# Performance work log

Hardware: AMD Instinct MI355X
Metric: run time of the kernel (lower is better)

The kernel has to match this reference:

```python
import jax, jax.numpy as jnp
import numpy as np
from jax import lax

B, T, I, H, L = 64, 512, 256, 512, 2


def setup_inputs() -> dict:
    key = jax.random.key(0)
    ks = jax.random.split(key, 5)
    s_in = (6.0 / (H + I)) ** 0.5   # xavier-uniform-like scale
    s_hh = (6.0 / (H + H)) ** 0.5
    return {
        "x": jax.random.normal(ks[0], (B, T, I), jnp.float32),
        "h_0": jnp.zeros((L, B, H), jnp.float32),
        "W_ih_0": jax.random.normal(ks[1], (H, I), jnp.float32) * s_in,
        "W_hh_0": jax.random.normal(ks[2], (H, H), jnp.float32) * s_hh,
        "b_ih_0": jnp.zeros((H,), jnp.float32),
        "b_hh_0": jnp.zeros((H,), jnp.float32),
        "W_ih_1": jax.random.normal(ks[3], (H, H), jnp.float32) * s_hh,
        "W_hh_1": jax.random.normal(ks[4], (H, H), jnp.float32) * s_hh,
        "b_ih_1": jnp.zeros((H,), jnp.float32),
        "b_hh_1": jnp.zeros((H,), jnp.float32),
    }


def _rnn_layer(xs, h0, W_ih, W_hh, b_ih, b_hh):
    # Precompute the input-to-hidden projection for all timesteps at once
    # (same math as per-step F.linear, just batched): [B,T,H]
    xW = jnp.einsum('bti,hi->bth', xs, W_ih) + b_ih + b_hh

    def step(h, xw_t):  # h:[B,H], xw_t:[B,H]
        h_new = jnp.tanh(xw_t + h @ W_hh.T)
        return h_new, h_new

    h_last, ys = lax.scan(step, h0, jnp.swapaxes(xW, 0, 1))  # ys: [T,B,H]
    return jnp.swapaxes(ys, 0, 1), h_last


def reference(x, h_0, W_ih_0, W_hh_0, b_ih_0, b_hh_0,
              W_ih_1, W_hh_1, b_ih_1, b_hh_1):
    out0, h_n0 = _rnn_layer(x, h_0[0], W_ih_0, W_hh_0, b_ih_0, b_hh_0)
    out1, h_n1 = _rnn_layer(out0, h_0[1], W_ih_1, W_hh_1, b_ih_1, b_hh_1)
    h_n = jnp.stack([h_n0, h_n1], axis=0)  # [L,B,H]
    return out1, h_n
```

## Files before the change

kernel.cpp:

```cpp
#include <hip/hip_runtime.h>


#define kB 64
#define kT 512
#define kI 256
#define kH 512
#define kBH (kB * kH)

typedef _Float16 half8 __attribute__((ext_vector_type(8)));
typedef float floatx4 __attribute__((ext_vector_type(4)));

constexpr size_t W16_B   = 0;
constexpr size_t OUT0M_B = 16u * 1024 * 1024;
constexpr size_t H1M_B   = OUT0M_B + (size_t)(kT + 1) * kBH * 2;
constexpr size_t CNT_B   = H1M_B + (size_t)(kT + 1) * kBH * 2;

__device__ inline half8 cvt8(const float* p) {
    const float4* p4 = (const float4*)p;
    float4 a = p4[0], b = p4[1];
    half8 h;
    h[0] = (_Float16)a.x; h[1] = (_Float16)a.y; h[2] = (_Float16)a.z; h[3] = (_Float16)a.w;
    h[4] = (_Float16)b.x; h[5] = (_Float16)b.y; h[6] = (_Float16)b.z; h[7] = (_Float16)b.w;
    return h;
}

__device__ inline void sc_store_half(_Float16* p, _Float16 v) {
    unsigned short u = __builtin_bit_cast(unsigned short, v);
    __hip_atomic_store((unsigned short*)p, u, __ATOMIC_RELAXED, __HIP_MEMORY_SCOPE_AGENT);
}

__device__ inline void wait_slot(const int* p, int target) {
    int guard = 0;
    while (__hip_atomic_load(p, __ATOMIC_RELAXED, __HIP_MEMORY_SCOPE_AGENT) < target)
        if (++guard > 100000000) break;
    asm volatile("" ::: "memory");
}

__device__ inline void wait_pair(const int* slots, int target) {
    const int* p = slots + (threadIdx.x & 1);
    int guard = 0;
    for (;;) {
        int v = __hip_atomic_load(p, __ATOMIC_RELAXED, __HIP_MEMORY_SCOPE_AGENT);
        if (__all(v >= target)) break;
        if (++guard > 100000000) break;
    }
    asm volatile("" ::: "memory");
}

__device__ inline void wait_quarters(const int* slots, int own, int target) {
    const int idx = threadIdx.x & 3;
    const int* p = slots + idx;
    int guard = 0;
    for (;;) {
        int v = (idx == own) ? target
              : __hip_atomic_load(p, __ATOMIC_RELAXED, __HIP_MEMORY_SCOPE_AGENT);
        if (__all(v >= target)) break;
        if (++guard > 100000000) break;
    }
    asm volatile("" ::: "memory");
}

__global__ void setup_kernel(const float* __restrict__ h0, const float* __restrict__ wih0,
                             _Float16* __restrict__ out0m, _Float16* __restrict__ h1m,
                             _Float16* __restrict__ w16, int* __restrict__ cnt) {
    int idx = blockIdx.x * blockDim.x + threadIdx.x;
    if (idx < kBH) out0m[idx] = (_Float16)h0[idx];
    else if (idx < 2 * kBH) h1m[idx - kBH] = (_Float16)h0[idx];
    w16[idx] = (_Float16)wih0[idx];
    if (idx < 256) cnt[idx] = 0;
}

__global__ __launch_bounds__(256) void xw_kernel(
    const float* __restrict__ x, const _Float16* __restrict__ w16,
    const float* __restrict__ bih, const float* __restrict__ bhh, float* xw) {
    const int mb = blockIdx.x >> 3, nb = blockIdx.x & 7;
    const int wave = threadIdx.x >> 6, lane = threadIdx.x & 63;
    const int r = lane & 15, q = lane >> 4;
    const int m0 = mb * 64 + wave * 16;
    half8 a[8];
#pragma unroll
    for (int ko = 0; ko < 8; ++ko)
        a[ko] = cvt8(x + (size_t)(m0 + r) * kI + ko * 32 + q * 8);
#pragma unroll
    for (int ct = 0; ct < 4; ++ct) {
        const int cc = nb * 64 + ct * 16 + r;
        const float bias = bih[cc] + bhh[cc];
        floatx4 acc = {bias, bias, bias, bias};
#pragma unroll
        for (int ko = 0; ko < 8; ++ko) {
            half8 b = *(const half8*)(w16 + (size_t)cc * kI + ko * 32 + q * 8);
            acc = __builtin_amdgcn_mfma_f32_16x16x32_f16(a[ko], b, acc, 0, 0, 0);
        }
#pragma unroll
        for (int j = 0; j < 4; ++j)
            xw[(size_t)(m0 + q * 4 + j) * kH + cc] = acc[j];
    }
}

__global__ __launch_bounds__(1024) void scan_kernel(
    const float* xw,
    _Float16* __restrict__ out0m, _Float16* __restrict__ h1m,
    int* __restrict__ slots0, int* __restrict__ slots1,
    float* out1,
    const float* __restrict__ whh0,
    const float* __restrict__ wih1, const float* __restrict__ whh1,
    const float* __restrict__ bih1, const float* __restrict__ bhh1) {
    __shared__ __align__(16) char smem[40960];

    const int blk = blockIdx.x;
    const int tid = threadIdx.x;
    const int wave = tid >> 6, lane = tid & 63;
    const int r = lane & 15, q = lane >> 4;
    const int rb = (r << 10), swz = (r & 7) << 4;

    if (blk < 8) {
        const int g = blk >> 1, half = blk & 1;
        const int b0 = g * 16;
        const int cc = half * 256 + wave * 16 + r;
        half8 wfh[16];
#pragma unroll
        for (int ks = 0; ks < 16; ++ks)
            wfh[ks] = cvt8(whh0 + (size_t)cc * kH + ks * 32 + q * 8);
        int* myslot = slots0 + g * 2 + half;
        const int* peerslot = slots0 + g * 2 + (half ^ 1);
        const int srow = tid >> 6, sunit = tid & 63;
        const size_t sg_off = (size_t)(b0 + srow) * kH + sunit * 8;
        char* sdst = smem + (((srow << 10) | (sunit << 4)) ^ ((srow & 7) << 4));

        for (int t = 0; t < kT; ++t) {
            float xwv[4];
#pragma unroll
            for (int j = 0; j < 4; ++j)
                xwv[j] = xw[((size_t)(b0 + q * 4 + j) * kT + t) * kH + cc];
            if (t > 0) wait_slot(peerslot, t);
            *(half8*)sdst = *(const half8*)(out0m + (size_t)t * kBH + sg_off);
            __syncthreads();
            floatx4 acc = {0.f, 0.f, 0.f, 0.f};
#pragma unroll
            for (int ks = 0; ks < 16; ++ks) {
                half8 la = *(const half8*)(smem + ((rb | (ks << 6) | (q << 4)) ^ swz));
                acc = __builtin_amdgcn_mfma_f32_16x16x32_f16(la, wfh[ks], acc, 0, 0, 0);
            }
            _Float16* dst = out0m + (size_t)(t + 1) * kBH + (size_t)(b0 + q * 4) * kH + cc;
#pragma unroll
            for (int j = 0; j < 4; ++j)
                sc_store_half(dst + (size_t)j * kH, (_Float16)tanhf(acc[j] + xwv[j]));
            asm volatile("" ::: "memory");
            __builtin_amdgcn_s_waitcnt(0x0F70);
            __syncthreads();
            if (tid == 0)
                __hip_atomic_store(myslot, t + 1, __ATOMIC_RELAXED, __HIP_MEMORY_SCOPE_AGENT);
        }
    } else {
        const int b2 = blk - 8;
        const int g = b2 >> 2, qb = b2 & 3;
        const int b0 = g * 16;
        const int ct = wave >> 1, part = wave & 1;
        const int cc = qb * 128 + ct * 16 + r;
        half8 wf[16];
        const float* wsrc = part ? wih1 : whh1;
#pragma unroll
        for (int ks = 0; ks < 16; ++ks)
            wf[ks] = cvt8(wsrc + (size_t)cc * kH + ks * 32 + q * 8);
        const float bias = (part == 0) ? (bih1[cc] + bhh1[cc]) : 0.f;
        int* myslot = slots1 + g * 4 + qb;
        const int* gq = slots1 + g * 4;
        const int* gh = slots0 + g * 2;
        const int u = ct * 64 + lane;
        const int srow = u >> 5, sunit = u & 31;
        const size_t sg_off = (size_t)(b0 + srow) * kH + sunit * 16;
        const int tbase = part ? 16384 : 0;
        char* sd0 = smem + tbase + ((((srow << 10) | (sunit << 5))) ^ ((srow & 7) << 4));
        char* sd1 = smem + tbase + ((((srow << 10) | (sunit << 5)) | 16) ^ ((srow & 7) << 4));
        float* redp = (float*)(smem + 32768) + (ct * 256 + lane * 4);

        for (int t = 0; t < kT; ++t) {
            const _Float16* sl;
            if (part == 0) {
                if (t > 0) wait_quarters(gq, qb, t);
                sl = h1m + (size_t)t * kBH;
            } else {
                wait_pair(gh, t + 1);
                sl = out0m + (size_t)(t + 1) * kBH;
            }
            half8 s0 = *(const half8*)(sl + sg_off);
            half8 s1 = *(const half8*)(sl + sg_off + 8);
            *(half8*)sd0 = s0;
            *(half8*)sd1 = s1;
            __syncthreads();
            floatx4 acc = {0.f, 0.f, 0.f, 0.f};
            const char* tb = smem + tbase;
#pragma unroll
            for (int ks = 0; ks < 16; ++ks) {
                half8 la = *(const half8*)(tb + ((rb | (ks << 6) | (q << 4)) ^ swz));
                acc = __builtin_amdgcn_mfma_f32_16x16x32_f16(la, wf[ks], acc, 0, 0, 0);
            }
            if (part == 1) *(floatx4*)redp = acc;
            __syncthreads();
            if (part == 0) {
                floatx4 o = *(const floatx4*)redp;
#pragma unroll
                for (int j = 0; j < 4; ++j) {
                    float v = tanhf(acc[j] + o[j] + bias);
                    out1[((size_t)(b0 + q * 4 + j) * kT + t) * kH + cc] = v;
                    sc_store_half(h1m + (size_t)(t + 1) * kBH + (size_t)(b0 + q * 4 + j) * kH + cc,
                                  (_Float16)v);
                }
            }
            asm volatile("" ::: "memory");
            __builtin_amdgcn_s_waitcnt(0x0F70);
            __syncthreads();
            if (tid == 0)
                __hip_atomic_store(myslot, t + 1, __ATOMIC_RELAXED, __HIP_MEMORY_SCOPE_AGENT);
        }
    }
}

__global__ void finalize_kernel(const _Float16* __restrict__ out0m,
                                const _Float16* __restrict__ h1m,
                                float* __restrict__ out) {
    int idx = blockIdx.x * blockDim.x + threadIdx.x;
    float* hn = out + (size_t)kB * kT * kH;
    if (idx < kBH) hn[idx] = (float)out0m[(size_t)kT * kBH + idx];
    else hn[idx] = (float)h1m[(size_t)kT * kBH + (idx - kBH)];
}

extern "C" void kernel_launch(void* const* d_in, const int* in_sizes, int n_in,
                              void* d_out, int out_size, void* d_ws, size_t ws_size,
                              hipStream_t stream) {
    const float* x    = (const float*)d_in[0];
    const float* h0in = (const float*)d_in[1];
    const float* wih0 = (const float*)d_in[2];
    const float* whh0 = (const float*)d_in[3];
    const float* bih0 = (const float*)d_in[4];
    const float* bhh0 = (const float*)d_in[5];
    const float* wih1 = (const float*)d_in[6];
    const float* whh1 = (const float*)d_in[7];
    const float* bih1 = (const float*)d_in[8];
    const float* bhh1 = (const float*)d_in[9];
    float* out = (float*)d_out;
    char* ws = (char*)d_ws;

    _Float16* w16   = (_Float16*)(ws + W16_B);
    _Float16* out0m = (_Float16*)(ws + OUT0M_B);
    _Float16* h1m   = (_Float16*)(ws + H1M_B);
    int* cnt        = (int*)(ws + CNT_B);
    int* slots0 = cnt;
    int* slots1 = cnt + 32;

    setup_kernel<<<512, 256, 0, stream>>>(h0in, wih0, out0m, h1m, w16, cnt);
    xw_kernel<<<4096, 256, 0, stream>>>(x, w16, bih0, bhh0, out);
    scan_kernel<<<24, 1024, 0, stream>>>(out, out0m, h1m, slots0, slots1, out,
                                         whh0, wih1, whh1, bih1, bhh1);
    finalize_kernel<<<256, 256, 0, stream>>>(out0m, h1m, out);
}
```

Before: 2.046 ms.

## Replace counter-slot handshakes with sentinel-polled LLC loads and double-buffered LDS state

Removes the per-step atomic slot counters and barriers used to signal progress between workgroups. Hidden-state buffers are pre-filled with an all-ones sentinel, and consumers poll the data itself through cache-bypassing loads until no sentinel remains. Each workgroup keeps its own half or quarter of the state in double-buffered LDS, so only the peer's portion is fetched from memory, and block size is halved with each wave computing more columns. Also switches to an exp-based tanh and pre-converts the weights to fp16 in setup. This risks subtle memory-ordering bugs, and a legitimate fp16 value of 0xFFFF would never occur, but NaN-like patterns could stall polling.

```diff
diff --git a/kernel.cpp b/kernel.cpp
--- a/kernel.cpp
+++ b/kernel.cpp
@@ -9,11 +9,63 @@
 
 typedef _Float16 half8 __attribute__((ext_vector_type(8)));
 typedef float floatx4 __attribute__((ext_vector_type(4)));
+typedef unsigned u32x4 __attribute__((ext_vector_type(4)));
+typedef unsigned u32x2 __attribute__((ext_vector_type(2)));
+
+#define MFMA(a, b, c) __builtin_amdgcn_mfma_f32_16x16x32_f16(a, b, c, 0, 0, 0)
 
 constexpr size_t W16_B   = 0;
-constexpr size_t OUT0M_B = 16u * 1024 * 1024;
+constexpr size_t WH0_B   = 256u * 1024;
+constexpr size_t WI1_B   = WH0_B + 512u * 1024;
+constexpr size_t WH1_B   = WI1_B + 512u * 1024;
+constexpr size_t OUT0M_B = 2u * 1024 * 1024;
 constexpr size_t H1M_B   = OUT0M_B + (size_t)(kT + 1) * kBH * 2;
-constexpr size_t CNT_B   = H1M_B + (size_t)(kT + 1) * kBH * 2;
+
+__device__ inline void llc_store16(void* p, u32x4 v) {
+    asm volatile("global_store_dwordx4 %0, %1, off sc0 sc1" :: "v"(p), "v"(v) : "memory");
+}
+__device__ inline void llc_store8(void* p, u32x2 v) {
+    asm volatile("global_store_dwordx2 %0, %1, off sc0 sc1" :: "v"(p), "v"(v) : "memory");
+}
+#define LLC_ISSUE16(dst, p) \
+    asm volatile("global_load_dwordx4 %0, %1, off sc0 sc1" : "=v"(dst) : "v"(p))
+
+__device__ inline unsigned dirty4(u32x4 v) {
+    unsigned m01 = v[0] > v[1] ? v[0] : v[1];
+    unsigned m23 = v[2] > v[3] ? v[2] : v[3];
+    unsigned m = m01 > m23 ? m01 : m23;
+    return m == 0xFFFFFFFFu;
+}
+
+__device__ inline float fast_tanh(float x) {
+    float e = __expf(2.f * x);
+    return 1.f - 2.f / (e + 1.f);
+}
+
+__global__ void setup_kernel(const float* __restrict__ h0,
+                             const float* __restrict__ wih0, const float* __restrict__ whh0,
+                             const float* __restrict__ wih1, const float* __restrict__ whh1,
+                             _Float16* __restrict__ w16, _Float16* __restrict__ wh0_16,
+                             _Float16* __restrict__ wi1_16, _Float16* __restrict__ wh1_16,
+                             _Float16* __restrict__ out0m, _Float16* __restrict__ h1m) {
+    size_t tid = (size_t)blockIdx.x * blockDim.x + threadIdx.x;
+    size_t stride = (size_t)gridDim.x * blockDim.x;
+    for (size_t i = tid; i < (size_t)kH * kI; i += stride) w16[i] = (_Float16)wih0[i];
+    for (size_t i = tid; i < (size_t)kH * kH; i += stride) {
+        wh0_16[i] = (_Float16)whh0[i];
+        wi1_16[i] = (_Float16)wih1[i];
+        wh1_16[i] = (_Float16)whh1[i];
+    }
+    for (size_t i = tid; i < kBH; i += stride) {
+        out0m[i] = (_Float16)h0[i];
+        h1m[i]   = (_Float16)h0[kBH + i];
+    }
+    u32x4 s = {0xFFFFFFFFu, 0xFFFFFFFFu, 0xFFFFFFFFu, 0xFFFFFFFFu};
+    u32x4* a = (u32x4*)(out0m + kBH);
+    u32x4* b = (u32x4*)(h1m + kBH);
+    const size_t nf = (size_t)kT * kBH / 8;
+    for (size_t i = tid; i < nf; i += stride) { a[i] = s; b[i] = s; }
+}
 
 __device__ inline half8 cvt8(const float* p) {
     const float4* p4 = (const float4*)p;
@@ -22,52 +74,6 @@
     h[0] = (_Float16)a.x; h[1] = (_Float16)a.y; h[2] = (_Float16)a.z; h[3] = (_Float16)a.w;
     h[4] = (_Float16)b.x; h[5] = (_Float16)b.y; h[6] = (_Float16)b.z; h[7] = (_Float16)b.w;
     return h;
-}
-
-__device__ inline void sc_store_half(_Float16* p, _Float16 v) {
-    unsigned short u = __builtin_bit_cast(unsigned short, v);
-    __hip_atomic_store((unsigned short*)p, u, __ATOMIC_RELAXED, __HIP_MEMORY_SCOPE_AGENT);
-}
-
-__device__ inline void wait_slot(const int* p, int target) {
-    int guard = 0;
-    while (__hip_atomic_load(p, __ATOMIC_RELAXED, __HIP_MEMORY_SCOPE_AGENT) < target)
-        if (++guard > 100000000) break;
-    asm volatile("" ::: "memory");
-}
-
-__device__ inline void wait_pair(const int* slots, int target) {
-    const int* p = slots + (threadIdx.x & 1);
-    int guard = 0;
-    for (;;) {
-        int v = __hip_atomic_load(p, __ATOMIC_RELAXED, __HIP_MEMORY_SCOPE_AGENT);
-        if (__all(v >= target)) break;
-        if (++guard > 100000000) break;
-    }
-    asm volatile("" ::: "memory");
-}
-
-__device__ inline void wait_quarters(const int* slots, int own, int target) {
-    const int idx = threadIdx.x & 3;
-    const int* p = slots + idx;
-    int guard = 0;
-    for (;;) {
-        int v = (idx == own) ? target
-              : __hip_atomic_load(p, __ATOMIC_RELAXED, __HIP_MEMORY_SCOPE_AGENT);
-        if (__all(v >= target)) break;
-        if (++guard > 100000000) break;
-    }
-    asm volatile("" ::: "memory");
-}
-
-__global__ void setup_kernel(const float* __restrict__ h0, const float* __restrict__ wih0,
-                             _Float16* __restrict__ out0m, _Float16* __restrict__ h1m,
-                             _Float16* __restrict__ w16, int* __restrict__ cnt) {
-    int idx = blockIdx.x * blockDim.x + threadIdx.x;
-    if (idx < kBH) out0m[idx] = (_Float16)h0[idx];
-    else if (idx < 2 * kBH) h1m[idx - kBH] = (_Float16)h0[idx];
-    w16[idx] = (_Float16)wih0[idx];
-    if (idx < 256) cnt[idx] = 0;
 }
 
 __global__ __launch_bounds__(256) void xw_kernel(
@@ -89,7 +95,7 @@
 #pragma unroll
         for (int ko = 0; ko < 8; ++ko) {
             half8 b = *(const half8*)(w16 + (size_t)cc * kI + ko * 32 + q * 8);
-            acc = __builtin_amdgcn_mfma_f32_16x16x32_f16(a[ko], b, acc, 0, 0, 0);
+            acc = MFMA(a[ko], b, acc);
         }
 #pragma unroll
         for (int j = 0; j < 4; ++j)
@@ -97,121 +103,190 @@
     }
 }
 
-__global__ __launch_bounds__(1024) void scan_kernel(
+__global__ __launch_bounds__(512, 2) void scan_kernel(
     const float* xw,
     _Float16* __restrict__ out0m, _Float16* __restrict__ h1m,
-    int* __restrict__ slots0, int* __restrict__ slots1,
     float* out1,
-    const float* __restrict__ whh0,
-    const float* __restrict__ wih1, const float* __restrict__ whh1,
+    const _Float16* __restrict__ wh0_16,
+    const _Float16* __restrict__ wi1_16, const _Float16* __restrict__ wh1_16,
     const float* __restrict__ bih1, const float* __restrict__ bhh1) {
-    __shared__ __align__(16) char smem[40960];
+    __shared__ __align__(16) char smem[24576];
 
     const int blk = blockIdx.x;
     const int tid = threadIdx.x;
     const int wave = tid >> 6, lane = tid & 63;
     const int r = lane & 15, q = lane >> 4;
-    const int rb = (r << 10), swz = (r & 7) << 4;
+    const int swzr = (r & 7) << 4;
+    const int srow = tid >> 5, sl32 = tid & 31;
+    const int swzs = (srow & 7) << 4;
 
     if (blk < 8) {
         const int g = blk >> 1, half = blk & 1;
         const int b0 = g * 16;
-        const int cc = half * 256 + wave * 16 + r;
-        half8 wfh[16];
-#pragma unroll
-        for (int ks = 0; ks < 16; ++ks)
-            wfh[ks] = cvt8(whh0 + (size_t)cc * kH + ks * 32 + q * 8);
-        int* myslot = slots0 + g * 2 + half;
-        const int* peerslot = slots0 + g * 2 + (half ^ 1);
-        const int srow = tid >> 6, sunit = tid & 63;
-        const size_t sg_off = (size_t)(b0 + srow) * kH + sunit * 8;
-        char* sdst = smem + (((srow << 10) | (sunit << 4)) ^ ((srow & 7) << 4));
+        const int cb = half * 256 + wave * 32;
+        half8 wf0[16], wf1[16];
+#pragma unroll
+        for (int ks = 0; ks < 16; ++ks) {
+            wf0[ks] = *(const half8*)(wh0_16 + (size_t)(cb + r) * kH + ks * 32 + q * 8);
+            wf1[ks] = *(const half8*)(wh0_16 + (size_t)(cb + 16 + r) * kH + ks * 32 + q * 8);
+        }
+        {
+            u32x4 v = *(const u32x4*)(out0m + (size_t)(b0 + srow) * kH + half * 256 + sl32 * 8);
+            *(u32x4*)(smem + srow * 512 + ((sl32 * 16) ^ swzs)) = v;
+        }
+        __syncthreads();
 
         for (int t = 0; t < kT; ++t) {
-            float xwv[4];
-#pragma unroll
-            for (int j = 0; j < 4; ++j)
-                xwv[j] = xw[((size_t)(b0 + q * 4 + j) * kT + t) * kH + cc];
-            if (t > 0) wait_slot(peerslot, t);
-            *(half8*)sdst = *(const half8*)(out0m + (size_t)t * kBH + sg_off);
+            char* bufR = smem + (t & 1) * 8192;
+            char* bufW = smem + ((t + 1) & 1) * 8192;
+            float xv0[4], xv1[4];
+#pragma unroll
+            for (int j = 0; j < 4; ++j) {
+                const size_t rowb = ((size_t)(b0 + q * 4 + j) * kT + t) * kH;
+                xv0[j] = xw[rowb + cb + r];
+                xv1[j] = xw[rowb + cb + 16 + r];
+            }
+            u32x4 ph[8];
+            const _Float16* pb = out0m + (size_t)t * kBH + (size_t)(b0 + r) * kH
+                                 + (half ^ 1) * 256 + q * 8;
+#pragma unroll
+            for (int i = 0; i < 8; ++i) LLC_ISSUE16(ph[i], pb + i * 32);
+            floatx4 a0 = {0.f, 0.f, 0.f, 0.f}, a1 = {0.f, 0.f, 0.f, 0.f};
+#pragma unroll
+            for (int i = 0; i < 8; ++i) {
+                half8 la = *(const half8*)(bufR + r * 512 + ((i * 64 + q * 16) ^ swzr));
+                a0 = MFMA(la, wf0[half * 8 + i], a0);
+                a1 = MFMA(la, wf1[half * 8 + i], a1);
+            }
+            {
+                int guard = 0;
+                for (;;) {
+                    __builtin_amdgcn_s_waitcnt(0x0F70);
+                    __builtin_amdgcn_sched_barrier(0);
+                    unsigned d = 0;
+#pragma unroll
+                    for (int i = 0; i < 8; ++i) d |= dirty4(ph[i]);
+                    if (!__any(d != 0)) break;
+                    if (++guard > (1 << 20)) break;
+#pragma unroll
+                    for (int i = 0; i < 8; ++i) LLC_ISSUE16(ph[i], pb + i * 32);
+                }
+            }
+#pragma unroll
+            for (int i = 0; i < 8; ++i) {
+                half8 pa = __builtin_bit_cast(half8, ph[i]);
+                a0 = MFMA(pa, wf0[(half ^ 1) * 8 + i], a0);
+                a1 = MFMA(pa, wf1[(half ^ 1) * 8 + i], a1);
+            }
+#pragma unroll
+            for (int j = 0; j < 4; ++j) {
+                float v0 = fast_tanh(a0[j] + xv0[j]);
+                float v1 = fast_tanh(a1[j] + xv1[j]);
+                const int row = q * 4 + j;
+                const int sz = (row & 7) << 4;
+                *(_Float16*)(bufW + row * 512 + (((wave * 32 + r) * 2) ^ sz)) = (_Float16)v0;
+                *(_Float16*)(bufW + row * 512 + (((wave * 32 + 16 + r) * 2) ^ sz)) = (_Float16)v1;
+            }
             __syncthreads();
-            floatx4 acc = {0.f, 0.f, 0.f, 0.f};
-#pragma unroll
-            for (int ks = 0; ks < 16; ++ks) {
-                half8 la = *(const half8*)(smem + ((rb | (ks << 6) | (q << 4)) ^ swz));
-                acc = __builtin_amdgcn_mfma_f32_16x16x32_f16(la, wfh[ks], acc, 0, 0, 0);
-            }
-            _Float16* dst = out0m + (size_t)(t + 1) * kBH + (size_t)(b0 + q * 4) * kH + cc;
-#pragma unroll
-            for (int j = 0; j < 4; ++j)
-                sc_store_half(dst + (size_t)j * kH, (_Float16)tanhf(acc[j] + xwv[j]));
-            asm volatile("" ::: "memory");
-            __builtin_amdgcn_s_waitcnt(0x0F70);
-            __syncthreads();
-            if (tid == 0)
-                __hip_atomic_store(myslot, t + 1, __ATOMIC_RELAXED, __HIP_MEMORY_SCOPE_AGENT);
+            u32x4 sv = *(const u32x4*)(bufW + srow * 512 + ((sl32 * 16) ^ swzs));
+            llc_store16(out0m + (size_t)(t + 1) * kBH + (size_t)(b0 + srow) * kH
+                        + half * 256 + sl32 * 8, sv);
         }
     } else {
         const int b2 = blk - 8;
         const int g = b2 >> 2, qb = b2 & 3;
         const int b0 = g * 16;
-        const int ct = wave >> 1, part = wave & 1;
-        const int cc = qb * 128 + ct * 16 + r;
-        half8 wf[16];
-        const float* wsrc = part ? wih1 : whh1;
-#pragma unroll
-        for (int ks = 0; ks < 16; ++ks)
-            wf[ks] = cvt8(wsrc + (size_t)cc * kH + ks * 32 + q * 8);
-        const float bias = (part == 0) ? (bih1[cc] + bhh1[cc]) : 0.f;
-        int* myslot = slots1 + g * 4 + qb;
-        const int* gq = slots1 + g * 4;
-        const int* gh = slots0 + g * 2;
-        const int u = ct * 64 + lane;
-        const int srow = u >> 5, sunit = u & 31;
-        const size_t sg_off = (size_t)(b0 + srow) * kH + sunit * 16;
-        const int tbase = part ? 16384 : 0;
-        char* sd0 = smem + tbase + ((((srow << 10) | (sunit << 5))) ^ ((srow & 7) << 4));
-        char* sd1 = smem + tbase + ((((srow << 10) | (sunit << 5)) | 16) ^ ((srow & 7) << 4));
-        float* redp = (float*)(smem + 32768) + (ct * 256 + lane * 4);
+        const int c0 = qb * 128 + wave * 16;
+        half8 wfh[16], wfi[16];
+#pragma unroll
+        for (int ks = 0; ks < 16; ++ks) {
+            wfh[ks] = *(const half8*)(wh1_16 + (size_t)(c0 + r) * kH + ks * 32 + q * 8);
+            wfi[ks] = *(const half8*)(wi1_16 + (size_t)(c0 + r) * kH + ks * 32 + q * 8);
+        }
+        const float bias = bih1[c0 + r] + bhh1[c0 + r];
+        char* h1b = smem;
+        char* o1b = smem + 8192;
+        {
+            u32x2 v = *(const u32x2*)(h1m + (size_t)(b0 + srow) * kH + qb * 128 + sl32 * 4);
+            *(u32x2*)(h1b + srow * 256 + ((sl32 * 8) ^ swzs)) = v;
+        }
+        __syncthreads();
 
         for (int t = 0; t < kT; ++t) {
-            const _Float16* sl;
-            if (part == 0) {
-                if (t > 0) wait_quarters(gq, qb, t);
-                sl = h1m + (size_t)t * kBH;
-            } else {
-                wait_pair(gh, t + 1);
-                sl = out0m + (size_t)(t + 1) * kBH;
-            }
-            half8 s0 = *(const half8*)(sl + sg_off);
-            half8 s1 = *(const half8*)(sl + sg_off + 8);
-            *(half8*)sd0 = s0;
-            *(half8*)sd1 = s1;
+            char* bR = h1b + (t & 1) * 4096;
+            char* bW = h1b + ((t + 1) & 1) * 4096;
+            char* oW = o1b + (t & 1) * 8192;
+            floatx4 a0 = {0.f, 0.f, 0.f, 0.f}, a1 = {0.f, 0.f, 0.f, 0.f};
+            u32x4 hp[12];
+            const _Float16* hb = h1m + (size_t)t * kBH + (size_t)(b0 + r) * kH + q * 8;
+#pragma unroll
+            for (int i = 0; i < 12; ++i) {
+                const int ks = i + (i >= qb * 4 ? 4 : 0);
+                LLC_ISSUE16(hp[i], hb + ks * 32);
+            }
+#pragma unroll
+            for (int i = 0; i < 4; ++i) {
+                half8 la = *(const half8*)(bR + r * 256 + ((i * 64 + q * 16) ^ swzr));
+                a0 = MFMA(la, wfh[qb * 4 + i], a0);
+            }
+            {
+                int guard = 0;
+                for (;;) {
+                    __builtin_amdgcn_s_waitcnt(0x0F70);
+                    __builtin_amdgcn_sched_barrier(0);
+                    unsigned d = 0;
+#pragma unroll
+                    for (int i = 0; i < 12; ++i) d |= dirty4(hp[i]);
+                    if (!__any(d != 0)) break;
+                    if (++guard > (1 << 20)) break;
+#pragma unroll
+                    for (int i = 0; i < 12; ++i) {
+                        const int ks = i + (i >= qb * 4 ? 4 : 0);
+                        LLC_ISSUE16(hp[i], hb + ks * 32);
+                    }
+                }
+            }
+#pragma unroll
+            for (int i = 0; i < 12; ++i) {
+                const int ks = i + (i >= qb * 4 ? 4 : 0);
+                a0 = MFMA(__builtin_bit_cast(half8, hp[i]), wfh[ks], a0);
+            }
+            u32x4 xp[16];
+            const _Float16* xb = out0m + (size_t)(t + 1) * kBH + (size_t)(b0 + r) * kH + q * 8;
+#pragma unroll
+            for (int i = 0; i < 16; ++i) LLC_ISSUE16(xp[i], xb + i * 32);
+            {
+                int guard = 0;
+                for (;;) {
+                    __builtin_amdgcn_s_waitcnt(0x0F70);
+                    __builtin_amdgcn_sched_barrier(0);
+                    unsigned d = 0;
+#pragma unroll
+                    for (int i = 0; i < 16; ++i) d |= dirty4(xp[i]);
+                    if (!__any(d != 0)) break;
+                    if (++guard > (1 << 20)) break;
+#pragma unroll
+                    for (int i = 0; i < 16; ++i) LLC_ISSUE16(xp[i], xb + i * 32);
+                }
+            }
+#pragma unroll
+            for (int i = 0; i < 16; ++i)
+                a1 = MFMA(__builtin_bit_cast(half8, xp[i]), wfi[i], a1);
+#pragma unroll
+            for (int j = 0; j < 4; ++j) {
+                float v = fast_tanh(a0[j] + a1[j] + bias);
+                const int row = q * 4 + j;
+                const int sz = (row & 7) << 4;
+                const int cl = wave * 16 + r;
+                *(_Float16*)(bW + row * 256 + ((cl * 2) ^ sz)) = (_Float16)v;
+                *(float*)(oW + row * 512 + ((cl * 4) ^ sz)) = v;
+            }
             __syncthreads();
-            floatx4 acc = {0.f, 0.f, 0.f, 0.f};
-            const char* tb = smem + tbase;
-#pragma unroll
-            for (int ks = 0; ks < 16; ++ks) {
-                half8 la = *(const half8*)(tb + ((rb | (ks << 6) | (q << 4)) ^ swz));
-                acc = __builtin_amdgcn_mfma_f32_16x16x32_f16(la, wf[ks], acc, 0, 0, 0);
-            }
-            if (part == 1) *(floatx4*)redp = acc;
-            __syncthreads();
-            if (part == 0) {
-                floatx4 o = *(const floatx4*)redp;
-#pragma unroll
-                for (int j = 0; j < 4; ++j) {
-                    float v = tanhf(acc[j] + o[j] + bias);
-                    out1[((size_t)(b0 + q * 4 + j) * kT + t) * kH + cc] = v;
-                    sc_store_half(h1m + (size_t)(t + 1) * kBH + (size_t)(b0 + q * 4 + j) * kH + cc,
-                                  (_Float16)v);
-                }
-            }
-            asm volatile("" ::: "memory");
-            __builtin_amdgcn_s_waitcnt(0x0F70);
-            __syncthreads();
-            if (tid == 0)
-                __hip_atomic_store(myslot, t + 1, __ATOMIC_RELAXED, __HIP_MEMORY_SCOPE_AGENT);
+            u32x2 hv = *(const u32x2*)(bW + srow * 256 + ((sl32 * 8) ^ swzs));
+            llc_store8(h1m + (size_t)(t + 1) * kBH + (size_t)(b0 + srow) * kH
+                       + qb * 128 + sl32 * 4, hv);
+            u32x4 ov = *(const u32x4*)(oW + srow * 512 + ((sl32 * 16) ^ swzs));
+            *(u32x4*)(out1 + ((size_t)(b0 + srow) * kT + t) * kH + qb * 128 + sl32 * 4) = ov;
         }
     }
 }
@@ -241,16 +316,17 @@
     float* out = (float*)d_out;
     char* ws = (char*)d_ws;
 
-    _Float16* w16   = (_Float16*)(ws + W16_B);
-    _Float16* out0m = (_Float16*)(ws + OUT0M_B);
-    _Float16* h1m   = (_Float16*)(ws + H1M_B);
-    int* cnt        = (int*)(ws + CNT_B);
-    int* slots0 = cnt;
-    int* slots1 = cnt + 32;
-
-    setup_kernel<<<512, 256, 0, stream>>>(h0in, wih0, out0m, h1m, w16, cnt);
+    _Float16* w16    = (_Float16*)(ws + W16_B);
+    _Float16* wh0_16 = (_Float16*)(ws + WH0_B);
+    _Float16* wi1_16 = (_Float16*)(ws + WI1_B);
+    _Float16* wh1_16 = (_Float16*)(ws + WH1_B);
+    _Float16* out0m  = (_Float16*)(ws + OUT0M_B);
+    _Float16* h1m    = (_Float16*)(ws + H1M_B);
+
+    setup_kernel<<<2048, 256, 0, stream>>>(h0in, wih0, whh0, wih1, whh1,
+                                           w16, wh0_16, wi1_16, wh1_16, out0m, h1m);
     xw_kernel<<<4096, 256, 0, stream>>>(x, w16, bih0, bhh0, out);
-    scan_kernel<<<24, 1024, 0, stream>>>(out, out0m, h1m, slots0, slots1, out,
-                                         whh0, wih1, whh1, bih1, bhh1);
+    scan_kernel<<<24, 512, 0, stream>>>(out, out0m, h1m, out,
+                                        wh0_16, wi1_16, wh1_16, bih1, bhh1);
     finalize_kernel<<<256, 256, 0, stream>>>(out0m, h1m, out);
 }
```

Result: slower. 5.553 ms (+171.4%).
